# Kernel tuning notes

Measured on AMD Instinct MI355X. Metric: run time of the kernel, lower is better.

Reference implementation:

```python
import jax, jax.numpy as jnp
import numpy as np

OUT_CH = 19  # out_channels


def setup_inputs() -> dict:
    key = jax.random.key(0)
    ks = jax.random.split(key, 8)
    N1, N2, C = 8000, 8000, 96
    return {
        "sur_sv_feature": jax.random.normal(ks[0], (N2, C), jnp.float32),
        "sur_sv_coords": jax.random.uniform(ks[1], (N2, 3), jnp.float32, -20.0, 20.0),
        "sur_sv_gt": jax.random.randint(ks[2], (N2,), 0, OUT_CH, dtype=jnp.int32),
        "sv_prob": jax.random.normal(ks[3], (N1, OUT_CH), jnp.float32),
        "mean_features": jax.random.normal(ks[4], (N1, C), jnp.float32),
        "ori_coords": jax.random.uniform(ks[5], (N1, 3), jnp.float32, -20.0, 20.0),
        # well-conditioned invertible 4x4 homogeneous poses
        "posses": jnp.eye(4, dtype=jnp.float32)[None, :, :] + 0.05 * jax.random.normal(ks[6], (2, 4, 4), jnp.float32),
        "sv_gt_idx": jax.random.randint(ks[7], (N2,), 0, N1, dtype=jnp.int32),  # unused in forward
        "lg": 8000,
    }


def _alignment(coords, posses):
    # rev=1 branch: diff = inv(poses[1]) @ poses[0]; aligned = (diff @ [coords,1]^T)^T[:, :3]
    diff = jnp.linalg.inv(posses[1]) @ posses[0]
    homo = jnp.concatenate([coords, jnp.ones((coords.shape[0], 1), coords.dtype)], axis=1)
    return (homo @ diff.T)[:, :3]


def reference(sur_sv_feature, sur_sv_coords, sur_sv_gt, sv_prob, mean_features, ori_coords, posses, sv_gt_idx, lg):
    N1 = sv_prob.shape[0]
    al = _alignment(sur_sv_coords, posses)  # [N2,3]
    # cosine distance [N1,N2]
    w1 = jnp.linalg.norm(mean_features, axis=1, keepdims=True)
    w2 = jnp.linalg.norm(sur_sv_feature, axis=1, keepdims=True)
    feat_dist_cos = 1.0 - (mean_features @ sur_sv_feature.T) / jnp.maximum(w1 * w2.T, 1e-8)
    # squared L2 distance [N1,N2], scaled by 1/0.5^2
    xn = jnp.sum(ori_coords ** 2, axis=1)[:, None]
    yn = jnp.sum(al ** 2, axis=1)[None, :]
    coords_dist = jnp.maximum(xn + yn - 2.0 * (ori_coords @ al.T), 0.0) / 0.25
    support = (coords_dist < 100.0).astype(jnp.float32)  # 10**2 radius gate
    onehot = jnp.eye(OUT_CH, dtype=jnp.float32)[sur_sv_gt]  # [N2,19]
    dist_matric = 1.0 + feat_dist_cos - jnp.exp(-0.5 * coords_dist)
    K = jnp.exp(-dist_matric / 0.03) * support
    # 'Sinkhorn' loop: b,a depend only on constants u1,u2, so each of the 10
    # iterations computes identical values -> compute once (bit-identical).
    u2 = jnp.full((K.shape[0],), 1.0 / K.shape[0], jnp.float32)
    u1 = jnp.full((K.shape[1],), 1.0 / K.shape[1], jnp.float32)
    b = u2 / (K @ u1 + 1e-16)      # [N1]
    a = u1 / (K.T @ u2 + 1e-16)    # [N2]
    # diag(a) @ K.T @ diag(b) = a[:,None] * K.T * b[None,:]  -> [N2,N1]
    sim = (a[:, None] * K.T) * b[None, :]
    sim = sim[:lg]
    sv_prob_updated = jax.nn.softmax(sv_prob, axis=1)
    sm_index = jnp.argmax(sim, axis=1)          # [lg] indices into N1
    tmpx = sur_sv_gt[:lg]                       # onehot[:lg].argmax == gt labels
    vals = sv_prob_updated[sm_index, tmpx]      # diag(P[sm_index].index_select(1,tmpx))
    mask = jnp.where(jnp.any(vals > 0.1), vals > 0.1, vals > 0.0)
    scatter_idx = jnp.where(mask, sm_index, N1)  # out-of-bounds sentinel -> dropped
    sv_prob_new = sv_prob_updated.at[scatter_idx].set(onehot[:lg], mode='drop')
    # torch.unique(sm_index[tmp]); padded with -1 for jit-static shape
    trust = jnp.unique(jnp.where(mask, sm_index, -1), size=lg, fill_value=-1)
    pre = jnp.argmax(sv_prob_new, axis=1)
    return (trust, mean_features, ori_coords, pre, sv_prob_new, trust)
```

## Files before the change

### kernel.cpp

```cpp
#include <hip/hip_runtime.h>

#define N 8000
#define C4 24
#define OCH 19
#define NCELL 1000
#define NCH 32
#define HSZ (NCH*NCELL)
#define U1 (1.0f/8000.0f)
#define PAIR_CAP 256
#define NREP 8

__device__ __forceinline__ int clamp10(int v) { return min(max(v, 0), 9); }

__global__ void __launch_bounds__(256) k_prep(
    const float* __restrict__ sf, const float* __restrict__ coords,
    const float* __restrict__ posses,
    float* __restrict__ w2, float4* __restrict__ alN,
    int* __restrict__ cellB, int* __restrict__ histB,
    int4* __restrict__ ck4, int4* __restrict__ wn4, int* __restrict__ flags) {
    int bx = blockIdx.x, tid = threadIdx.x;
    if (bx < 32) {
        __shared__ int lhist[NCELL];
        __shared__ float sdiff[12];
        for (int c = tid; c < NCELL; c += 256) lhist[c] = 0;
        int j = bx*256 + tid;
        if (tid == 0) {
            double M[4][8];
            for (int r = 0; r < 4; ++r)
                for (int c = 0; c < 4; ++c) {
                    M[r][c] = (double)posses[16 + r*4 + c];
                    M[r][4+c] = (r == c) ? 1.0 : 0.0;
                }
            for (int col = 0; col < 4; ++col) {
                int piv = col; double best = fabs(M[col][col]);
                for (int r = col+1; r < 4; ++r) { double v = fabs(M[r][col]); if (v > best) { best = v; piv = r; } }
                if (piv != col) for (int c = 0; c < 8; ++c) { double t = M[col][c]; M[col][c] = M[piv][c]; M[piv][c] = t; }
                double inv = 1.0 / M[col][col];
                for (int c = 0; c < 8; ++c) M[col][c] *= inv;
                for (int r = 0; r < 4; ++r) if (r != col) {
                    double f = M[r][col];
                    for (int c = 0; c < 8; ++c) M[r][c] -= f * M[col][c];
                }
            }
            for (int r = 0; r < 3; ++r)
                for (int c = 0; c < 4; ++c) {
                    double sm = 0.0;
                    for (int k = 0; k < 4; ++k) sm += M[r][4+k] * (double)posses[k*4 + c];
                    sdiff[r*4 + c] = (float)sm;
                }
        }
        __syncthreads();
        if (j < N) {
            float c0 = coords[j*3], c1 = coords[j*3+1], c2 = coords[j*3+2];
            float a0 = (sdiff[0]*c0 + sdiff[1]*c1) + (sdiff[2]*c2 + sdiff[3]);
            float a1 = (sdiff[4]*c0 + sdiff[5]*c1) + (sdiff[6]*c2 + sdiff[7]);
            float a2 = (sdiff[8]*c0 + sdiff[9]*c1) + (sdiff[10]*c2 + sdiff[11]);
            alN[j] = make_float4(a0, a1, a2, a0*a0 + a1*a1 + a2*a2);
            int cx = clamp10((int)floorf((a0 + 25.f) * 0.2f));
            int cy = clamp10((int)floorf((a1 + 25.f) * 0.2f));
            int cz = clamp10((int)floorf((a2 + 25.f) * 0.2f));
            int cc = (cz*10 + cy)*10 + cx;
            cellB[j] = cc;
            atomicAdd(&lhist[cc], 1);
        }
        __syncthreads();
        for (int c = tid; c < NCELL; c += 256) histB[bx*NCELL + c] = lhist[c];
    } else if (bx < 64) {
        int b = bx - 32;
        int u = tid & 3;
        #pragma unroll
        for (int p0 = 0; p0 < 256; p0 += 64) {
            int jp = b*256 + p0 + (tid >> 2);
            float ax = 0.f, ay = 0.f, az = 0.f, aw = 0.f;
            if (jp < N) {
                const float4* s4 = (const float4*)sf + jp*C4;
                #pragma unroll
                for (int s2 = 0; s2 < 6; ++s2) {
                    float4 v = s4[s2*4 + u];
                    ax += v.x*v.x; ay += v.y*v.y; az += v.z*v.z; aw += v.w*v.w;
                }
            }
            float pp = (ax + ay) + (az + aw);
            pp += __shfl_xor(pp, 1);
            pp += __shfl_xor(pp, 2);
            if (jp < N && u == 0) w2[jp] = sqrtf(pp);
        }
    } else {
        int t0 = (bx-64)*256 + tid;
        int4 z = make_int4(0, 0, 0, 0);
        int4 f = make_int4(-1, -1, -1, -1);
        for (int t = t0; t < 36000; t += 16*256) {
            if (t < 32000) ck4[t] = z;
            else wn4[t-32000] = f;
        }
        if (bx == 64 && tid < 8) flags[tid] = 0;
    }
}

__global__ void __launch_bounds__(256) k_scatter(
    const int* __restrict__ cellB, const int* __restrict__ h,
    const float* __restrict__ w2, const float4* __restrict__ alN,
    int* __restrict__ idBR, float* __restrict__ w2R, float4* __restrict__ alR,
    int* __restrict__ csB) {
    __shared__ int sStart[NCELL];
    __shared__ int wtot[4];
    __shared__ int sc[256];
    int chunk = blockIdx.x, tid = threadIdx.x;

    int tot0 = 0, tot1 = 0, tot2 = 0, tot3 = 0;
    int pre0 = 0, pre1 = 0, pre2 = 0, pre3 = 0;
    bool cv = tid < 250;
    if (cv) {
        for (int ch = 0; ch < NCH; ++ch) {
            int4 v = ((const int4*)(h + ch*NCELL))[tid];
            tot0 += v.x; tot1 += v.y; tot2 += v.z; tot3 += v.w;
            if (ch < chunk) { pre0 += v.x; pre1 += v.y; pre2 += v.z; pre3 += v.w; }
        }
    }
    int S = tot0 + tot1 + tot2 + tot3;
    int lane = tid & 63, wv = tid >> 6;
    int x = S;
    for (int off = 1; off < 64; off <<= 1) { int y = __shfl_up(x, off); if (lane >= off) x += y; }
    if (lane == 63) wtot[wv] = x;
    __syncthreads();
    int wpre = 0;
    for (int k = 0; k < 4; ++k) if (k < wv) wpre += wtot[k];
    int run = wpre + x - S;
    if (cv) {
        int c = tid*4;
        sStart[c]   = run + pre0; if (chunk == 0) csB[c]   = run; run += tot0;
        sStart[c+1] = run + pre1; if (chunk == 0) csB[c+1] = run; run += tot1;
        sStart[c+2] = run + pre2; if (chunk == 0) csB[c+2] = run; run += tot2;
        sStart[c+3] = run + pre3; if (chunk == 0) csB[c+3] = run; run += tot3;
    }
    if (chunk == 0 && tid == 0) csB[NCELL] = N;

    int gi = chunk*256 + tid;
    int cell = (gi < N) ? cellB[gi] : -1;
    sc[tid] = cell;
    __syncthreads();
    if (gi >= N) return;
    int rank = 0;
    const int4* sc4 = (const int4*)sc;
    int full = tid >> 2;
    for (int t4 = 0; t4 < full; ++t4) {
        int4 q = sc4[t4];
        rank += (q.x == cell) + (q.y == cell) + (q.z == cell) + (q.w == cell);
    }
    for (int t = full*4; t < tid; ++t) rank += (sc[t] == cell);
    int pos = sStart[cell] + rank;
    idBR[pos] = gi;
    w2R[pos] = w2[gi];
    alR[pos] = alN[gi];
}

__global__ void __launch_bounds__(256) k_pairs(
    const float4* __restrict__ mf4, const float* __restrict__ ori,
    const float4* __restrict__ alR, const float* __restrict__ w2R,
    const float4* __restrict__ sf4, const int* __restrict__ idBR,
    const int* __restrict__ csB,
    unsigned long long* __restrict__ colkeyR) {
    __shared__ float4 sRow[4][C4];
    __shared__ int bgi[4][128];
    __shared__ float bc[4][128];
    __shared__ float bw[4][128];
    __shared__ int sJ[4][PAIR_CAP];
    __shared__ float sK[4][PAIR_CAP];

    int tid = threadIdx.x, lane = tid & 63, w = tid >> 6;
    int i = blockIdx.x * 4 + w;
    if (lane < C4) sRow[w][lane] = mf4[i*C4 + lane];
    __syncthreads();

    float ox = ori[i*3], oy = ori[i*3+1], oz = ori[i*3+2];
    float xnv = ox*ox + oy*oy + oz*oz;
    float s = 0.f;
    for (int kk = 0; kk < C4; ++kk) {
        float4 v = sRow[w][kk];
        s += v.x*v.x; s += v.y*v.y; s += v.z*v.z; s += v.w*v.w;
    }
    float w1v = sqrtf(s);

    int cx = clamp10((int)floorf((ox + 25.f) * 0.2f));
    int cy = clamp10((int)floorf((oy + 25.f) * 0.2f));
    int cz = clamp10((int)floorf((oz + 25.f) * 0.2f));
    int xlo = max(cx-1, 0), xhi = min(cx+1, 9);

    int s_[9], l_[9], c_[9];
    int tot = 0;
    #pragma unroll
    for (int t = 0; t < 9; ++t) {
        int z = cz + (t/3) - 1, y = cy + (t%3) - 1;
        bool ok = ((unsigned)z <= 9u) && ((unsigned)y <= 9u);
        int ss = 0, ee = 0;
        if (ok) {
            int cbase = (z*10 + y)*10;
            ss = csB[cbase + xlo];
            ee = csB[cbase + xhi + 1];
        }
        s_[t] = ss; l_[t] = ee - ss; c_[t] = tot; tot += ee - ss;
    }

    auto calcq = [&](int f) -> int {
        int q = 0;
        #pragma unroll
        for (int t = 0; t < 9; ++t) {
            bool in = (f >= c_[t]) && (f - c_[t] < l_[t]);
            if (in) q = s_[t] + (f - c_[t]);
        }
        return q;
    };

    int cnt = 0, done = 0, npairs = 0;
    float racc = 0.f;
    unsigned long long lmask = (lane == 0) ? 0ull : (~0ull >> (64 - lane));
    int gu = lane & 3, gt_ = lane >> 2;

    auto process16 = [&](int nb) {
        int slot = (done + gt_) & 127;
        int gi = bgi[w][slot];
        float cdb = bc[w][slot];
        float w2v = bw[w][slot];
        float dotp = 0.f;
        if (gt_ < nb) {
            const float4* br = sf4 + gi*C4;
            float ax = 0.f, ay = 0.f, az = 0.f, aw = 0.f;
            #pragma unroll
            for (int s2 = 0; s2 < 6; ++s2) {
                int kk = s2*4 + gu;
                float4 a = sRow[w][kk];
                float4 b = br[kk];
                ax += a.x*b.x; ay += a.y*b.y; az += a.z*b.z; aw += a.w*b.w;
            }
            dotp = (ax + ay) + (az + aw);
        }
        dotp += __shfl_xor(dotp, 1);
        dotp += __shfl_xor(dotp, 2);
        if (gt_ < nb && gu == 0) {
            float fdc = 1.f - dotp / fmaxf(w1v * w2v, 1e-8f);
            float dist = (1.f + fdc) - expf(-0.5f * cdb);
            float K = expf(-dist / 0.03f);
            racc += K * U1;
            int sl = npairs + gt_;
            if (sl < PAIR_CAP) { sJ[w][sl] = gi; sK[w][sl] = K; }
        }
        npairs += nb;
        done += nb;
    };

    bool act_cur = lane < tot;
    float4 aj_cur = make_float4(0.f, 0.f, 0.f, 0.f);
    int gi_cur = 0; float w2_cur = 0.f;
    if (act_cur) {
        int q = calcq(lane);
        aj_cur = alR[q]; gi_cur = idBR[q]; w2_cur = w2R[q];
    }
    for (int f0 = 0; f0 < tot; f0 += 64) {
        int fn = f0 + 64 + lane;
        bool act_n = fn < tot;
        float4 aj_n = make_float4(0.f, 0.f, 0.f, 0.f);
        int gi_n = 0; float w2_n = 0.f;
        if (act_n) {
            int qn = calcq(fn);
            aj_n = alR[qn]; gi_n = idBR[qn]; w2_n = w2R[qn];
        }
        bool pass = false; float cdv = 0.f;
        if (act_cur) {
            float d = xnv + aj_cur.w - 2.f*(ox*aj_cur.x + oy*aj_cur.y + oz*aj_cur.z);
            cdv = fmaxf(d, 0.f) * 4.f;
            pass = cdv < 100.f;
        }
        unsigned long long m = __ballot(pass);
        if (pass) {
            int slot = (cnt + __popcll(m & lmask)) & 127;
            bgi[w][slot] = gi_cur; bc[w][slot] = cdv; bw[w][slot] = w2_cur;
        }
        cnt += __popcll(m);
        if (cnt - done >= 64) {
            process16(16); process16(16); process16(16); process16(16);
        }
        aj_cur = aj_n; gi_cur = gi_n; w2_cur = w2_n; act_cur = act_n;
    }
    while (cnt > done) {
        int nb = cnt - done; if (nb > 16) nb = 16;
        process16(nb);
    }

    for (int off = 32; off; off >>= 1) racc += __shfl_xor(racc, off);
    float bi = U1 / (racc + 1e-16f);

    unsigned long long* ck = colkeyR + (size_t)(blockIdx.x & (NREP-1)) * N;
    unsigned long long ikey = (unsigned long long)(unsigned)(N - i);
    int np = min(npairs, PAIR_CAP);
    for (int t = lane; t < np; t += 64) {
        float v = sK[w][t] * bi;
        if (v > 0.f) {
            unsigned long long key = ((unsigned long long)__float_as_uint(v) << 32) | ikey;
            atomicMax(&ck[sJ[w][t]], key);
        }
    }
}

__global__ void k_post(const unsigned long long* __restrict__ colkeyR,
                       const float* __restrict__ sv_prob, const int* __restrict__ gt,
                       int* __restrict__ winnerHi, int* __restrict__ winnerLo,
                       int* __restrict__ flags) {
    int j = blockIdx.x * 256 + threadIdx.x;
    int lane = threadIdx.x & 63;
    bool valid = j < N;
    float vv = 0.f; int bidx = 0;
    if (valid) {
        unsigned long long key = 0ull;
        #pragma unroll
        for (int r = 0; r < NREP; ++r) {
            unsigned long long k = colkeyR[(size_t)r*N + j];
            if (k > key) key = k;
        }
        bidx = key ? (N - (int)(key & 0xffffffffull)) : 0;
        const float* p = sv_prob + bidx*OCH;
        float m = -1e30f;
        for (int c = 0; c < OCH; ++c) m = fmaxf(m, p[c]);
        float ssum = 0.f, eg = 0.f; int g = gt[j];
        for (int c = 0; c < OCH; ++c) { float e = expf(p[c] - m); ssum += e; if (c == g) eg = e; }
        vv = eg / ssum;
    }
    bool hi = valid && (vv > 0.1f);
    bool nothi = valid && !(vv > 0.1f);
    bool lo = valid && (vv > 0.0f);
    bool notlo = valid && !(vv > 0.0f);
    if (hi) atomicMax(&winnerHi[bidx], j);
    if (lo) atomicMax(&winnerLo[bidx], j);
    unsigned long long m0 = __ballot(hi);
    unsigned long long m1 = __ballot(nothi);
    unsigned long long m2 = __ballot(notlo);
    if (lane == 0) {
        if (m0) atomicOr(&flags[0], 1);
        if (m1) atomicOr(&flags[1], 1);
        if (m2) atomicOr(&flags[2], 1);
    }
}

__global__ void __launch_bounds__(1024) k_final(
    const int* __restrict__ winnerHi, const int* __restrict__ winnerLo,
    const int* __restrict__ flags, const int* __restrict__ gt,
    const float* __restrict__ sv_prob,
    const float* __restrict__ mf, const float* __restrict__ ori,
    float* __restrict__ o_svp, float* __restrict__ o_pre,
    float* __restrict__ out0, float* __restrict__ out5,
    float* __restrict__ o_mf, float* __restrict__ o_ori) {
    int bx = blockIdx.x, tid = threadIdx.x;
    if (bx < 8) {
        const int* winner = flags[0] ? winnerHi : winnerLo;
        int i = bx*1024 + tid;
        if (i >= N) return;
        int w = winner[i];
        if (w >= 0) {
            int g = gt[w];
            for (int c = 0; c < OCH; ++c) o_svp[i*OCH + c] = (c == g) ? 1.f : 0.f;
            o_pre[i] = (float)g;
        } else {
            const float* p = sv_prob + i*OCH;
            float m = -1e30f;
            for (int c = 0; c < OCH; ++c) m = fmaxf(m, p[c]);
            float e[OCH]; float ssum = 0.f;
            for (int c = 0; c < OCH; ++c) { e[c] = expf(p[c] - m); ssum += e[c]; }
            float best = e[0] / ssum; int pidx = 0;
            o_svp[i*OCH] = best;
            for (int c = 1; c < OCH; ++c) {
                float r = e[c] / ssum;
                o_svp[i*OCH + c] = r;
                if (r > best) { best = r; pidx = c; }
            }
            o_pre[i] = (float)pidx;
        }
    } else if (bx == 8) {
        __shared__ int wsum[16];
        const int* winner = flags[0] ? winnerHi : winnerLo;
        int off = flags[0] ? (flags[1] ? 1 : 0) : (flags[2] ? 1 : 0);
        for (int p = tid; p < N; p += 1024) { out0[p] = -1.f; out5[p] = -1.f; }
        __syncthreads();
        int base = 0;
        for (int round = 0; round < N; round += 1024) {
            int i = round + tid;
            int pres = (i < N && winner[i] >= 0) ? 1 : 0;
            unsigned long long mask = __ballot(pres);
            int lane = tid & 63;
            int wv = tid >> 6;
            int excl = (lane == 0) ? 0 : __popcll(mask & (~0ull >> (64 - lane)));
            if (lane == 0) wsum[wv] = __popcll(mask);
            __syncthreads();
            int wpre = 0, tot = 0;
            for (int t = 0; t < 16; ++t) { if (t < wv) wpre += wsum[t]; tot += wsum[t]; }
            int pos = base + wpre + excl + off;
            if (pres && pos < N) { out0[pos] = (float)i; out5[pos] = (float)i; }
            base += tot;
            __syncthreads();
        }
    } else {
        const float4* mf4 = (const float4*)mf;
        const float4* ori4 = (const float4*)ori;
        float4* omf4 = (float4*)o_mf;
        float4* oori4 = (float4*)o_ori;
        int t0 = (bx-9)*1024 + tid;
        for (int t = t0; t < 198000; t += 51*1024) {
            if (t < 192000) omf4[t] = mf4[t];
            else oori4[t-192000] = ori4[t-192000];
        }
    }
}

extern "C" void kernel_launch(void* const* d_in, const int* in_sizes, int n_in,
                              void* d_out, int out_size, void* d_ws, size_t ws_size,
                              hipStream_t stream) {
    const float* sur_feat   = (const float*)d_in[0];
    const float* sur_coords = (const float*)d_in[1];
    const int*   sur_gt     = (const int*)d_in[2];
    const float* sv_prob    = (const float*)d_in[3];
    const float* mean_feat  = (const float*)d_in[4];
    const float* ori        = (const float*)d_in[5];
    const float* posses     = (const float*)d_in[6];

    float* out = (float*)d_out;
    float* o_trust  = out;
    float* o_mf     = out + 8000;
    float* o_ori    = out + 776000;
    float* o_pre    = out + 800000;
    float* o_svp    = out + 808000;
    float* o_trust2 = out + 960000;

    float* w = (float*)d_ws;
    float4* alN = (float4*)w;      w += 4*N;
    float4* alR = (float4*)w;      w += 4*N;
    unsigned long long* colkeyR = (unsigned long long*)w;  w += 2*NREP*N;
    float* w2 = w;                 w += N;
    float* w2R = w;                w += N;
    int* cellB = (int*)w;          w += N;
    int* histB = (int*)w;          w += HSZ;
    int* flags = (int*)w;          w += 8;
    int* csB = (int*)w;            w += 1008;
    int* idBR = (int*)w;           w += N;
    int* winnerHi = (int*)w;       w += N;
    int* winnerLo = (int*)w;       w += N;

    dim3 b256(256);

    k_prep<<<80, b256, 0, stream>>>(sur_feat, sur_coords, posses,
                                    w2, alN, cellB, histB,
                                    (int4*)colkeyR, (int4*)winnerHi, flags);
    k_scatter<<<32, b256, 0, stream>>>(cellB, histB, w2, alN, idBR, w2R, alR, csB);
    k_pairs<<<N/4, b256, 0, stream>>>((const float4*)mean_feat, ori, alR, w2R,
                                      (const float4*)sur_feat, idBR, csB, colkeyR);
    k_post<<<32, b256, 0, stream>>>(colkeyR, sv_prob, sur_gt, winnerHi, winnerLo, flags);
    k_final<<<60, 1024, 0, stream>>>(winnerHi, winnerLo, flags, sur_gt, sv_prob,
                                     mean_feat, ori,
                                     o_svp, o_pre, o_trust, o_trust2, o_mf, o_ori);
}
```

Before: 63.28 us.

## Bin query rows into supercells and reduce column maxima in LDS before global atomics

Query rows (ori coords) are now sorted into 5x5x5 supercells, and a new k_super kernel assigns each supercell to two 512-thread workgroups with an XCD-aware block remap. Each workgroup keeps a shared-memory table of per-column argmax keys for the 4x4x4 fine-cell neighbourhood, so most atomicMax operations hit LDS. Only the reduced keys are flushed to global colkeyR, with an overflow path for cells holding more than CELLCAP points. The aim is to cut global atomic contention and improve locality, at the cost of extra prep and scatter work and load imbalance across supercells.

```diff
diff --git a/kernel.cpp b/kernel.cpp
--- a/kernel.cpp
+++ b/kernel.cpp
@@ -4,19 +4,23 @@
 #define C4 24
 #define OCH 19
 #define NCELL 1000
+#define NC2 125
 #define NCH 32
 #define HSZ (NCH*NCELL)
 #define U1 (1.0f/8000.0f)
 #define PAIR_CAP 256
 #define NREP 8
+#define CELLCAP 40
+#define SCAP 2560
 
 __device__ __forceinline__ int clamp10(int v) { return min(max(v, 0), 9); }
 
 __global__ void __launch_bounds__(256) k_prep(
     const float* __restrict__ sf, const float* __restrict__ coords,
-    const float* __restrict__ posses,
+    const float* __restrict__ ori, const float* __restrict__ posses,
     float* __restrict__ w2, float4* __restrict__ alN,
     int* __restrict__ cellB, int* __restrict__ histB,
+    float4* __restrict__ oriN, int* __restrict__ cellA2, int* __restrict__ hist2,
     int4* __restrict__ ck4, int4* __restrict__ wn4, int* __restrict__ flags) {
     int bx = blockIdx.x, tid = threadIdx.x;
     if (bx < 32) {
@@ -66,7 +70,24 @@
         __syncthreads();
         for (int c = tid; c < NCELL; c += 256) histB[bx*NCELL + c] = lhist[c];
     } else if (bx < 64) {
-        int b = bx - 32;
+        __shared__ int lhist[NC2];
+        if (tid < NC2) lhist[tid] = 0;
+        __syncthreads();
+        int i = (bx-32)*256 + tid;
+        if (i < N) {
+            float ox = ori[i*3], oy = ori[i*3+1], oz = ori[i*3+2];
+            oriN[i] = make_float4(ox, oy, oz, ox*ox + oy*oy + oz*oz);
+            int cx = clamp10((int)floorf((ox + 25.f) * 0.2f));
+            int cy = clamp10((int)floorf((oy + 25.f) * 0.2f));
+            int cz = clamp10((int)floorf((oz + 25.f) * 0.2f));
+            int sc2 = (cz>>1)*25 + (cy>>1)*5 + (cx>>1);
+            cellA2[i] = sc2;
+            atomicAdd(&lhist[sc2], 1);
+        }
+        __syncthreads();
+        if (tid < NC2) hist2[(bx-32)*NC2 + tid] = lhist[tid];
+    } else if (bx < 96) {
+        int b = bx - 64;
         int u = tid & 3;
         #pragma unroll
         for (int p0 = 0; p0 < 256; p0 += 64) {
@@ -86,218 +107,315 @@
             if (jp < N && u == 0) w2[jp] = sqrtf(pp);
         }
     } else {
-        int t0 = (bx-64)*256 + tid;
+        int t0 = (bx-96)*256 + tid;
         int4 z = make_int4(0, 0, 0, 0);
         int4 f = make_int4(-1, -1, -1, -1);
         for (int t = t0; t < 36000; t += 16*256) {
             if (t < 32000) ck4[t] = z;
             else wn4[t-32000] = f;
         }
-        if (bx == 64 && tid < 8) flags[tid] = 0;
+        if (bx == 96 && tid < 8) flags[tid] = 0;
     }
 }
 
 __global__ void __launch_bounds__(256) k_scatter(
-    const int* __restrict__ cellB, const int* __restrict__ h,
-    const float* __restrict__ w2, const float4* __restrict__ alN,
-    int* __restrict__ idBR, float* __restrict__ w2R, float4* __restrict__ alR,
-    int* __restrict__ csB) {
+    const int* __restrict__ cellB, const int* __restrict__ histB,
+    const int* __restrict__ cellA2, const int* __restrict__ hist2,
+    const float* __restrict__ w2, const float4* __restrict__ alN, const float4* __restrict__ oriN,
+    int* __restrict__ idBR, float* __restrict__ w2R, float4* __restrict__ alR, int* __restrict__ csB,
+    int* __restrict__ idA2R, float4* __restrict__ oriA2R, int* __restrict__ csA2) {
     __shared__ int sStart[NCELL];
     __shared__ int wtot[4];
     __shared__ int sc[256];
-    int chunk = blockIdx.x, tid = threadIdx.x;
-
-    int tot0 = 0, tot1 = 0, tot2 = 0, tot3 = 0;
-    int pre0 = 0, pre1 = 0, pre2 = 0, pre3 = 0;
-    bool cv = tid < 250;
-    if (cv) {
-        for (int ch = 0; ch < NCH; ++ch) {
-            int4 v = ((const int4*)(h + ch*NCELL))[tid];
-            tot0 += v.x; tot1 += v.y; tot2 += v.z; tot3 += v.w;
-            if (ch < chunk) { pre0 += v.x; pre1 += v.y; pre2 += v.z; pre3 += v.w; }
-        }
-    }
-    int S = tot0 + tot1 + tot2 + tot3;
+    int bx = blockIdx.x, tid = threadIdx.x;
     int lane = tid & 63, wv = tid >> 6;
-    int x = S;
-    for (int off = 1; off < 64; off <<= 1) { int y = __shfl_up(x, off); if (lane >= off) x += y; }
-    if (lane == 63) wtot[wv] = x;
+
+    if (bx < 32) {
+        int chunk = bx;
+        int tot0 = 0, tot1 = 0, tot2 = 0, tot3 = 0;
+        int pre0 = 0, pre1 = 0, pre2 = 0, pre3 = 0;
+        bool cv = tid < 250;
+        if (cv) {
+            for (int ch = 0; ch < NCH; ++ch) {
+                int4 v = ((const int4*)(histB + ch*NCELL))[tid];
+                tot0 += v.x; tot1 += v.y; tot2 += v.z; tot3 += v.w;
+                if (ch < chunk) { pre0 += v.x; pre1 += v.y; pre2 += v.z; pre3 += v.w; }
+            }
+        }
+        int S = tot0 + tot1 + tot2 + tot3;
+        int x = S;
+        for (int off = 1; off < 64; off <<= 1) { int y = __shfl_up(x, off); if (lane >= off) x += y; }
+        if (lane == 63) wtot[wv] = x;
+        __syncthreads();
+        int wpre = 0;
+        for (int k = 0; k < 4; ++k) if (k < wv) wpre += wtot[k];
+        int run = wpre + x - S;
+        if (cv) {
+            int c = tid*4;
+            sStart[c]   = run + pre0; if (chunk == 0) csB[c]   = run; run += tot0;
+            sStart[c+1] = run + pre1; if (chunk == 0) csB[c+1] = run; run += tot1;
+            sStart[c+2] = run + pre2; if (chunk == 0) csB[c+2] = run; run += tot2;
+            sStart[c+3] = run + pre3; if (chunk == 0) csB[c+3] = run; run += tot3;
+        }
+        if (chunk == 0 && tid == 0) csB[NCELL] = N;
+
+        int gi = chunk*256 + tid;
+        int cell = (gi < N) ? cellB[gi] : -1;
+        sc[tid] = cell;
+        __syncthreads();
+        if (gi >= N) return;
+        int rank = 0;
+        const int4* sc4 = (const int4*)sc;
+        int full = tid >> 2;
+        for (int t4 = 0; t4 < full; ++t4) {
+            int4 q = sc4[t4];
+            rank += (q.x == cell) + (q.y == cell) + (q.z == cell) + (q.w == cell);
+        }
+        for (int t = full*4; t < tid; ++t) rank += (sc[t] == cell);
+        int pos = sStart[cell] + rank;
+        idBR[pos] = gi;
+        w2R[pos] = w2[gi];
+        alR[pos] = alN[gi];
+    } else {
+        int chunk = bx - 32;
+        int tot = 0, pre = 0;
+        if (tid < NC2) {
+            for (int ch = 0; ch < NCH; ++ch) {
+                int v = hist2[ch*NC2 + tid];
+                tot += v;
+                if (ch < chunk) pre += v;
+            }
+        }
+        int x = tot;
+        for (int off = 1; off < 64; off <<= 1) { int y = __shfl_up(x, off); if (lane >= off) x += y; }
+        if (lane == 63) wtot[wv] = x;
+        __syncthreads();
+        int wpre = 0;
+        for (int k = 0; k < 4; ++k) if (k < wv) wpre += wtot[k];
+        int base = wpre + x - tot;
+        if (tid < NC2) {
+            sStart[tid] = base + pre;
+            if (chunk == 0) csA2[tid] = base;
+        }
+        if (chunk == 0 && tid == 0) csA2[NC2] = N;
+
+        int gi = chunk*256 + tid;
+        int cell = (gi < N) ? cellA2[gi] : -1;
+        sc[tid] = cell;
+        __syncthreads();
+        if (gi >= N) return;
+        int rank = 0;
+        const int4* sc4 = (const int4*)sc;
+        int full = tid >> 2;
+        for (int t4 = 0; t4 < full; ++t4) {
+            int4 q = sc4[t4];
+            rank += (q.x == cell) + (q.y == cell) + (q.z == cell) + (q.w == cell);
+        }
+        for (int t = full*4; t < tid; ++t) rank += (sc[t] == cell);
+        int pos = sStart[cell] + rank;
+        idA2R[pos] = gi;
+        oriA2R[pos] = oriN[gi];
+    }
+}
+
+__global__ void __launch_bounds__(512) k_super(
+    const float4* __restrict__ mf4, const float4* __restrict__ sf4,
+    const float4* __restrict__ alR, const float* __restrict__ w2R,
+    const int* __restrict__ idBR, const int* __restrict__ csB,
+    const int* __restrict__ idA2R, const float4* __restrict__ oriA2R, const int* __restrict__ csA2,
+    unsigned long long* __restrict__ colkeyR) {
+    __shared__ unsigned long long sMax[SCAP];
+    __shared__ int   bgi[8][128];
+    __shared__ float bc[8][128];
+    __shared__ float bw[8][128];
+    __shared__ int   bf[8][128];
+    __shared__ int   listF[8][PAIR_CAP];
+    __shared__ float listK[8][PAIR_CAP];
+    __shared__ float4 sRow[8][C4];
+
+    int orig = blockIdx.x;
+    int xcd = orig & 7, idx = orig >> 3;
+    int wg = (xcd < 2 ? xcd*32 : 64 + (xcd-2)*31) + idx;
+    int sg = wg >> 1, half = wg & 1;
+    int rep = wg & (NREP-1);
+
+    int tid = threadIdx.x, lane = tid & 63, w = tid >> 6;
+    int rowBase = csA2[sg], rowEnd = csA2[sg+1];
+    if (rowBase >= rowEnd) return;
+
+    int sx = sg % 5, sy = (sg/5) % 5, sz = sg / 25;
+    int xlo_s = max(2*sx-1, 0);
+    int ylo_s = max(2*sy-1, 0);
+    int zlo_s = max(2*sz-1, 0);
+
+    for (int f = tid; f < SCAP; f += 512) sMax[f] = 0ull;
     __syncthreads();
-    int wpre = 0;
-    for (int k = 0; k < 4; ++k) if (k < wv) wpre += wtot[k];
-    int run = wpre + x - S;
-    if (cv) {
-        int c = tid*4;
-        sStart[c]   = run + pre0; if (chunk == 0) csB[c]   = run; run += tot0;
-        sStart[c+1] = run + pre1; if (chunk == 0) csB[c+1] = run; run += tot1;
-        sStart[c+2] = run + pre2; if (chunk == 0) csB[c+2] = run; run += tot2;
-        sStart[c+3] = run + pre3; if (chunk == 0) csB[c+3] = run; run += tot3;
-    }
-    if (chunk == 0 && tid == 0) csB[NCELL] = N;
-
-    int gi = chunk*256 + tid;
-    int cell = (gi < N) ? cellB[gi] : -1;
-    sc[tid] = cell;
-    __syncthreads();
-    if (gi >= N) return;
-    int rank = 0;
-    const int4* sc4 = (const int4*)sc;
-    int full = tid >> 2;
-    for (int t4 = 0; t4 < full; ++t4) {
-        int4 q = sc4[t4];
-        rank += (q.x == cell) + (q.y == cell) + (q.z == cell) + (q.w == cell);
-    }
-    for (int t = full*4; t < tid; ++t) rank += (sc[t] == cell);
-    int pos = sStart[cell] + rank;
-    idBR[pos] = gi;
-    w2R[pos] = w2[gi];
-    alR[pos] = alN[gi];
-}
-
-__global__ void __launch_bounds__(256) k_pairs(
-    const float4* __restrict__ mf4, const float* __restrict__ ori,
-    const float4* __restrict__ alR, const float* __restrict__ w2R,
-    const float4* __restrict__ sf4, const int* __restrict__ idBR,
-    const int* __restrict__ csB,
-    unsigned long long* __restrict__ colkeyR) {
-    __shared__ float4 sRow[4][C4];
-    __shared__ int bgi[4][128];
-    __shared__ float bc[4][128];
-    __shared__ float bw[4][128];
-    __shared__ int sJ[4][PAIR_CAP];
-    __shared__ float sK[4][PAIR_CAP];
-
-    int tid = threadIdx.x, lane = tid & 63, w = tid >> 6;
-    int i = blockIdx.x * 4 + w;
-    if (lane < C4) sRow[w][lane] = mf4[i*C4 + lane];
-    __syncthreads();
-
-    float ox = ori[i*3], oy = ori[i*3+1], oz = ori[i*3+2];
-    float xnv = ox*ox + oy*oy + oz*oz;
-    float s = 0.f;
-    for (int kk = 0; kk < C4; ++kk) {
-        float4 v = sRow[w][kk];
-        s += v.x*v.x; s += v.y*v.y; s += v.z*v.z; s += v.w*v.w;
-    }
-    float w1v = sqrtf(s);
-
-    int cx = clamp10((int)floorf((ox + 25.f) * 0.2f));
-    int cy = clamp10((int)floorf((oy + 25.f) * 0.2f));
-    int cz = clamp10((int)floorf((oz + 25.f) * 0.2f));
-    int xlo = max(cx-1, 0), xhi = min(cx+1, 9);
-
-    int s_[9], l_[9], c_[9];
-    int tot = 0;
-    #pragma unroll
-    for (int t = 0; t < 9; ++t) {
-        int z = cz + (t/3) - 1, y = cy + (t%3) - 1;
-        bool ok = ((unsigned)z <= 9u) && ((unsigned)y <= 9u);
-        int ss = 0, ee = 0;
-        if (ok) {
-            int cbase = (z*10 + y)*10;
-            ss = csB[cbase + xlo];
-            ee = csB[cbase + xhi + 1];
-        }
-        s_[t] = ss; l_[t] = ee - ss; c_[t] = tot; tot += ee - ss;
-    }
-
-    auto calcq = [&](int f) -> int {
-        int q = 0;
+
+    unsigned long long lmask = lane ? (~0ull >> (64 - lane)) : 0ull;
+    int gu = lane & 3, gt_ = lane >> 2;
+
+    for (int pos = rowBase + half*8 + w; pos < rowEnd; pos += 16) {
+        int giRow = idA2R[pos];
+        float4 o = oriA2R[pos];
+        if (lane < C4) sRow[w][lane] = mf4[giRow*C4 + lane];
+        asm volatile("s_waitcnt lgkmcnt(0) vmcnt(0)" ::: "memory");
+        float ssum = 0.f;
+        for (int kk = 0; kk < C4; ++kk) {
+            float4 v = sRow[w][kk];
+            ssum += v.x*v.x; ssum += v.y*v.y; ssum += v.z*v.z; ssum += v.w*v.w;
+        }
+        float w1v = sqrtf(ssum);
+
+        int cx = clamp10((int)floorf((o.x + 25.f) * 0.2f));
+        int cy = clamp10((int)floorf((o.y + 25.f) * 0.2f));
+        int cz = clamp10((int)floorf((o.z + 25.f) * 0.2f));
+        int xlo = max(cx-1, 0), xhi = min(cx+1, 9);
+
+        int s_[9], l_[9], c_[9], b1_[9], b2_[9], fb_[9];
+        int tot = 0;
         #pragma unroll
         for (int t = 0; t < 9; ++t) {
-            bool in = (f >= c_[t]) && (f - c_[t] < l_[t]);
-            if (in) q = s_[t] + (f - c_[t]);
-        }
-        return q;
-    };
-
-    int cnt = 0, done = 0, npairs = 0;
-    float racc = 0.f;
-    unsigned long long lmask = (lane == 0) ? 0ull : (~0ull >> (64 - lane));
-    int gu = lane & 3, gt_ = lane >> 2;
-
-    auto process16 = [&](int nb) {
-        int slot = (done + gt_) & 127;
-        int gi = bgi[w][slot];
-        float cdb = bc[w][slot];
-        float w2v = bw[w][slot];
-        float dotp = 0.f;
-        if (gt_ < nb) {
-            const float4* br = sf4 + gi*C4;
-            float ax = 0.f, ay = 0.f, az = 0.f, aw = 0.f;
+            int z = cz + (t/3) - 1, y = cy + (t%3) - 1;
+            bool ok = ((unsigned)z <= 9u) && ((unsigned)y <= 9u);
+            int ss = 0, ee = 0, bb1 = 0, bb2 = 0, fb = 0;
+            if (ok) {
+                int cbase = (z*10 + y)*10;
+                ss = csB[cbase + xlo];
+                ee = csB[cbase + xhi + 1];
+                bb1 = (xlo + 1 <= xhi) ? csB[cbase + xlo + 1] : ee;
+                bb2 = (xlo + 2 <= xhi) ? csB[cbase + xlo + 2] : ee;
+                fb = (((z - zlo_s)*4 + (y - ylo_s))*4 + (xlo - xlo_s)) * CELLCAP;
+            }
+            s_[t] = ss; l_[t] = ee - ss; c_[t] = tot; b1_[t] = bb1; b2_[t] = bb2; fb_[t] = fb;
+            tot += ee - ss;
+        }
+
+        auto calcq = [&](int f) -> int {
+            int q = 0;
             #pragma unroll
-            for (int s2 = 0; s2 < 6; ++s2) {
-                int kk = s2*4 + gu;
-                float4 a = sRow[w][kk];
-                float4 b = br[kk];
-                ax += a.x*b.x; ay += a.y*b.y; az += a.z*b.z; aw += a.w*b.w;
-            }
-            dotp = (ax + ay) + (az + aw);
-        }
-        dotp += __shfl_xor(dotp, 1);
-        dotp += __shfl_xor(dotp, 2);
-        if (gt_ < nb && gu == 0) {
-            float fdc = 1.f - dotp / fmaxf(w1v * w2v, 1e-8f);
-            float dist = (1.f + fdc) - expf(-0.5f * cdb);
-            float K = expf(-dist / 0.03f);
-            racc += K * U1;
-            int sl = npairs + gt_;
-            if (sl < PAIR_CAP) { sJ[w][sl] = gi; sK[w][sl] = K; }
-        }
-        npairs += nb;
-        done += nb;
-    };
-
-    bool act_cur = lane < tot;
-    float4 aj_cur = make_float4(0.f, 0.f, 0.f, 0.f);
-    int gi_cur = 0; float w2_cur = 0.f;
-    if (act_cur) {
-        int q = calcq(lane);
-        aj_cur = alR[q]; gi_cur = idBR[q]; w2_cur = w2R[q];
-    }
-    for (int f0 = 0; f0 < tot; f0 += 64) {
-        int fn = f0 + 64 + lane;
-        bool act_n = fn < tot;
-        float4 aj_n = make_float4(0.f, 0.f, 0.f, 0.f);
-        int gi_n = 0; float w2_n = 0.f;
-        if (act_n) {
-            int qn = calcq(fn);
-            aj_n = alR[qn]; gi_n = idBR[qn]; w2_n = w2R[qn];
-        }
-        bool pass = false; float cdv = 0.f;
+            for (int t = 0; t < 9; ++t) {
+                bool in = (f >= c_[t]) && (f - c_[t] < l_[t]);
+                if (in) q = s_[t] + (f - c_[t]);
+            }
+            return q;
+        };
+
+        int cnt = 0, done = 0, npairs = 0;
+        float racc = 0.f;
+
+        auto process16 = [&](int nb) {
+            int slot = (done + gt_) & 127;
+            int gi = bgi[w][slot];
+            float cdb = bc[w][slot];
+            float w2v = bw[w][slot];
+            int fenc = bf[w][slot];
+            float dotp = 0.f;
+            if (gt_ < nb) {
+                const float4* br = sf4 + gi*C4;
+                float ax = 0.f, ay = 0.f, az = 0.f, aw = 0.f;
+                #pragma unroll
+                for (int s2 = 0; s2 < 6; ++s2) {
+                    int kk = s2*4 + gu;
+                    float4 a = sRow[w][kk];
+                    float4 b = br[kk];
+                    ax += a.x*b.x; ay += a.y*b.y; az += a.z*b.z; aw += a.w*b.w;
+                }
+                dotp = (ax + ay) + (az + aw);
+            }
+            dotp += __shfl_xor(dotp, 1);
+            dotp += __shfl_xor(dotp, 2);
+            if (gt_ < nb && gu == 0) {
+                float fdc = 1.f - dotp / fmaxf(w1v * w2v, 1e-8f);
+                float dist = (1.f + fdc) - expf(-0.5f * cdb);
+                float K = expf(-dist / 0.03f);
+                racc += K * U1;
+                int sl = npairs + gt_;
+                if (sl < PAIR_CAP) { listF[w][sl] = fenc; listK[w][sl] = K; }
+            }
+            npairs += nb;
+            done += nb;
+        };
+
+        bool act_cur = lane < tot;
+        float4 aj_cur = make_float4(0.f, 0.f, 0.f, 0.f);
+        int gi_cur = 0, q_cur = 0; float w2_cur = 0.f;
         if (act_cur) {
-            float d = xnv + aj_cur.w - 2.f*(ox*aj_cur.x + oy*aj_cur.y + oz*aj_cur.z);
-            cdv = fmaxf(d, 0.f) * 4.f;
-            pass = cdv < 100.f;
-        }
-        unsigned long long m = __ballot(pass);
-        if (pass) {
-            int slot = (cnt + __popcll(m & lmask)) & 127;
-            bgi[w][slot] = gi_cur; bc[w][slot] = cdv; bw[w][slot] = w2_cur;
-        }
-        cnt += __popcll(m);
-        if (cnt - done >= 64) {
-            process16(16); process16(16); process16(16); process16(16);
-        }
-        aj_cur = aj_n; gi_cur = gi_n; w2_cur = w2_n; act_cur = act_n;
-    }
-    while (cnt > done) {
-        int nb = cnt - done; if (nb > 16) nb = 16;
-        process16(nb);
-    }
-
-    for (int off = 32; off; off >>= 1) racc += __shfl_xor(racc, off);
-    float bi = U1 / (racc + 1e-16f);
-
-    unsigned long long* ck = colkeyR + (size_t)(blockIdx.x & (NREP-1)) * N;
-    unsigned long long ikey = (unsigned long long)(unsigned)(N - i);
-    int np = min(npairs, PAIR_CAP);
-    for (int t = lane; t < np; t += 64) {
-        float v = sK[w][t] * bi;
-        if (v > 0.f) {
-            unsigned long long key = ((unsigned long long)__float_as_uint(v) << 32) | ikey;
-            atomicMax(&ck[sJ[w][t]], key);
-        }
+            q_cur = calcq(lane);
+            aj_cur = alR[q_cur]; gi_cur = idBR[q_cur]; w2_cur = w2R[q_cur];
+        }
+        for (int f0 = 0; f0 < tot; f0 += 64) {
+            int fn = f0 + 64 + lane;
+            bool act_n = fn < tot;
+            float4 aj_n = make_float4(0.f, 0.f, 0.f, 0.f);
+            int gi_n = 0, q_n = 0; float w2_n = 0.f;
+            if (act_n) {
+                q_n = calcq(fn);
+                aj_n = alR[q_n]; gi_n = idBR[q_n]; w2_n = w2R[q_n];
+            }
+            bool pass = false; float cdv = 0.f;
+            if (act_cur) {
+                float d = o.w + aj_cur.w - 2.f*(o.x*aj_cur.x + o.y*aj_cur.y + o.z*aj_cur.z);
+                cdv = fmaxf(d, 0.f) * 4.f;
+                pass = cdv < 100.f;
+            }
+            unsigned long long m = __ballot(pass);
+            if (pass) {
+                int fcur = f0 + lane;
+                int vb0 = 0, vb1 = 0, vb2 = 0, vfb = 0;
+                #pragma unroll
+                for (int t = 0; t < 9; ++t) {
+                    bool in = (fcur >= c_[t]) && (fcur - c_[t] < l_[t]);
+                    if (in) { vb0 = s_[t]; vb1 = b1_[t]; vb2 = b2_[t]; vfb = fb_[t]; }
+                }
+                int xi = (q_cur >= vb1) + (q_cur >= vb2);
+                int bsel = (xi == 0) ? vb0 : ((xi == 1) ? vb1 : vb2);
+                int rank = q_cur - bsel;
+                int fenc = (rank < CELLCAP) ? (vfb + xi*CELLCAP + rank) : (0x40000000 | q_cur);
+                int slot = (cnt + __popcll(m & lmask)) & 127;
+                bgi[w][slot] = gi_cur; bc[w][slot] = cdv; bw[w][slot] = w2_cur; bf[w][slot] = fenc;
+            }
+            cnt += __popcll(m);
+            if (cnt - done >= 64) {
+                process16(16); process16(16); process16(16); process16(16);
+            }
+            aj_cur = aj_n; gi_cur = gi_n; q_cur = q_n; w2_cur = w2_n; act_cur = act_n;
+        }
+        while (cnt > done) {
+            int nb = cnt - done; if (nb > 16) nb = 16;
+            process16(nb);
+        }
+
+        for (int off = 32; off; off >>= 1) racc += __shfl_xor(racc, off);
+        float bi = U1 / (racc + 1e-16f);
+
+        asm volatile("s_waitcnt lgkmcnt(0)" ::: "memory");
+        unsigned long long ikey = (unsigned long long)(unsigned)(N - giRow);
+        int np = min(npairs, PAIR_CAP);
+        for (int t = lane; t < np; t += 64) {
+            float v = listK[w][t] * bi;
+            if (v > 0.f) {
+                unsigned long long key = ((unsigned long long)__float_as_uint(v) << 32) | ikey;
+                int fenc = listF[w][t];
+                if (fenc & 0x40000000) {
+                    int q = fenc & 0x3fffffff;
+                    atomicMax(&colkeyR[(size_t)rep*N + idBR[q]], key);
+                } else {
+                    atomicMax(&sMax[fenc], key);
+                }
+            }
+        }
+    }
+    __syncthreads();
+
+    for (int f = tid; f < SCAP; f += 512) {
+        unsigned long long k = sMax[f];
+        if (!k) continue;
+        int lcell = f / CELLCAP;
+        int rank = f - lcell*CELLCAP;
+        int xrel = lcell & 3, yrel = (lcell >> 2) & 3, zrel = lcell >> 4;
+        int cell = ((zlo_s + zrel)*10 + (ylo_s + yrel))*10 + (xlo_s + xrel);
+        int q = csB[cell] + rank;
+        atomicMax(&colkeyR[(size_t)rep*N + idBR[q]], k);
     }
 }
 
@@ -430,26 +548,34 @@
 
     float* w = (float*)d_ws;
     float4* alN = (float4*)w;      w += 4*N;
+    float4* oriN = (float4*)w;     w += 4*N;
     float4* alR = (float4*)w;      w += 4*N;
+    float4* oriA2R = (float4*)w;   w += 4*N;
     unsigned long long* colkeyR = (unsigned long long*)w;  w += 2*NREP*N;
     float* w2 = w;                 w += N;
     float* w2R = w;                w += N;
     int* cellB = (int*)w;          w += N;
+    int* cellA2 = (int*)w;         w += N;
     int* histB = (int*)w;          w += HSZ;
+    int* hist2 = (int*)w;          w += NCH*NC2;
     int* flags = (int*)w;          w += 8;
     int* csB = (int*)w;            w += 1008;
+    int* csA2 = (int*)w;           w += 128;
     int* idBR = (int*)w;           w += N;
+    int* idA2R = (int*)w;          w += N;
     int* winnerHi = (int*)w;       w += N;
     int* winnerLo = (int*)w;       w += N;
 
     dim3 b256(256);
 
-    k_prep<<<80, b256, 0, stream>>>(sur_feat, sur_coords, posses,
-                                    w2, alN, cellB, histB,
-                                    (int4*)colkeyR, (int4*)winnerHi, flags);
-    k_scatter<<<32, b256, 0, stream>>>(cellB, histB, w2, alN, idBR, w2R, alR, csB);
-    k_pairs<<<N/4, b256, 0, stream>>>((const float4*)mean_feat, ori, alR, w2R,
-                                      (const float4*)sur_feat, idBR, csB, colkeyR);
+    k_prep<<<112, b256, 0, stream>>>(sur_feat, sur_coords, ori, posses,
+                                     w2, alN, cellB, histB,
+                                     oriN, cellA2, hist2,
+                                     (int4*)colkeyR, (int4*)winnerHi, flags);
+    k_scatter<<<64, b256, 0, stream>>>(cellB, histB, cellA2, hist2, w2, alN, oriN,
+                                       idBR, w2R, alR, csB, idA2R, oriA2R, csA2);
+    k_super<<<250, 512, 0, stream>>>((const float4*)mean_feat, (const float4*)sur_feat,
+                                     alR, w2R, idBR, csB, idA2R, oriA2R, csA2, colkeyR);
     k_post<<<32, b256, 0, stream>>>(colkeyR, sv_prob, sur_gt, winnerHi, winnerLo, flags);
     k_final<<<60, 1024, 0, stream>>>(winnerHi, winnerLo, flags, sur_gt, sv_prob,
                                      mean_feat, ori,
```

New measurement: 126.3 us. 99.7% more time.
